# Kernel optimization log

Measured on AMD Instinct MI355X. Metric: run time of the kernel, lower is better.

The kernel has to match this reference:

```python
import jax, jax.numpy as jnp
import numpy as np

N_HEADS = 8


def setup_inputs() -> dict:
    key = jax.random.key(0)
    qkv = jax.random.normal(key, (4, 1536, 2048), dtype=jnp.float32)
    return {"qkv": qkv}


def reference(qkv):
    bs, width, length = qkv.shape
    assert width % (3 * N_HEADS) == 0
    ch = width // (3 * N_HEADS)
    q, k, v = jnp.split(qkv, 3, axis=1)            # each [bs, H*C, T]
    scale = 1.0 / (ch ** 0.25)                      # 1/sqrt(sqrt(ch)) applied to both q and k
    q = (q * scale).reshape(bs * N_HEADS, ch, length)
    k = (k * scale).reshape(bs * N_HEADS, ch, length)
    v = v.reshape(bs * N_HEADS, ch, length)
    weight = jnp.einsum('bct,bcs->bts', q, k)       # [bs*H, T, T]
    weight = jax.nn.softmax(weight.astype(jnp.float32), axis=-1).astype(weight.dtype)
    a = jnp.einsum('bts,bcs->bct', weight, v)       # [bs*H, C, T]
    return a.reshape(bs, -1, length)
```

## Files before the change

### kernel.cpp

```cpp
#include <hip/hip_runtime.h>


typedef _Float16 half8  __attribute__((ext_vector_type(8)));
typedef _Float16 half4  __attribute__((ext_vector_type(4)));
typedef float    floatx4 __attribute__((ext_vector_type(4)));

constexpr int T   = 2048;
constexpr int TQ  = 128;
constexpr int TS  = 64;
constexpr int LDK = 72;
constexpr int LDV = 72;
constexpr int NIT = T / TS;
constexpr float QSCALE = 0.125f * 1.44269504088896340736f;

__device__ __forceinline__ half4 pack4(float a, float b, float c, float d) {
    half4 r;
    r[0] = (_Float16)a; r[1] = (_Float16)b;
    r[2] = (_Float16)c; r[3] = (_Float16)d;
    return r;
}

__global__ __launch_bounds__(512, 4)
void qkv_attn_kernel(const float* __restrict__ qkv, float* __restrict__ out) {
    __shared__ __align__(16) _Float16 sK[2][TS * LDK];
    __shared__ __align__(16) _Float16 sV[2][64 * LDV];

    const int tid  = threadIdx.x;
    const int wave = tid >> 6;
    const int lane = tid & 63;
    const int n16  = lane & 15;
    const int g    = lane >> 4;

    const int bx = blockIdx.x;
    const int h  = bx & 31;
    const int qt = bx >> 5;
    const int b  = h >> 3;
    const int hh = h & 7;
    const int q0 = qt * TQ;

    const float* __restrict__ qbase = qkv + (size_t)(b * 1536 + hh * 64) * T;
    const float* __restrict__ kbase = qkv + (size_t)(b * 1536 + 512 + hh * 64) * T;
    const float* __restrict__ vbase = qkv + (size_t)(b * 1536 + 1024 + hh * 64) * T;
    float* __restrict__ obase = out + (size_t)(b * 512 + hh * 64) * T;

    const bool producer = wave >= 4;

    const int ptid = tid & 255;
    const int ks   = ((ptid >> 6) << 4) | (ptid & 15);
    const int kc4  = ((ptid >> 4) & 3) << 2;
    const int vc   = ptid >> 4;
    const int vs4  = (ptid & 15) << 2;

    auto stage = [&](int buf, int s0) {
        _Float16* kd = &sK[buf][ks * LDK];
        const float* kg = kbase + s0 + ks;
#pragma unroll
        for (int i = 0; i < 4; ++i) {
            const int c = i * 16 + kc4;
            const float f0 = kg[(c + 0) * T];
            const float f1 = kg[(c + 1) * T];
            const float f2 = kg[(c + 2) * T];
            const float f3 = kg[(c + 3) * T];
            *(half4*)&kd[c] = pack4(f0, f1, f2, f3);
        }
        const float* vg = vbase + vc * T + s0 + vs4;
        _Float16* vd = &sV[buf][vc * LDV + vs4];
#pragma unroll
        for (int i = 0; i < 4; ++i) {
            const floatx4 vv = *(const floatx4*)&vg[i * 16 * T];
            *(half4*)&vd[i * 16 * LDV] = pack4(vv.x, vv.y, vv.z, vv.w);
        }
    };

    half8 bq[2][2];
    floatx4 oacc[4][2];
    float lsum[2];

    if (!producer) {
#pragma unroll
        for (int qt2 = 0; qt2 < 2; ++qt2) {
            const int q = q0 + wave * 32 + qt2 * 16 + n16;
#pragma unroll
            for (int kcA = 0; kcA < 2; ++kcA)
#pragma unroll
                for (int j = 0; j < 8; ++j) {
                    const int c = kcA * 32 + g * 8 + j;
                    bq[qt2][kcA][j] = (_Float16)(qbase[c * T + q] * QSCALE);
                }
        }
#pragma unroll
        for (int mt = 0; mt < 4; ++mt)
#pragma unroll
            for (int qt2 = 0; qt2 < 2; ++qt2) oacc[mt][qt2] = (floatx4)(0.f);
        lsum[0] = 0.f; lsum[1] = 0.f;
    }

    if (producer) stage(0, 0);
    __syncthreads();

    for (int it = 0; it < NIT; ++it) {
        const int buf = it & 1;
        if (producer) {
            if (it + 1 < NIT) stage(buf ^ 1, (it + 1) * TS);
        } else {
            const _Float16* kb = &sK[buf][0];
            const _Float16* vb = &sV[buf][0];
#pragma unroll
            for (int kc2 = 0; kc2 < 2; ++kc2) {
                floatx4 sacc[2][2];
#pragma unroll
                for (int sub = 0; sub < 2; ++sub) {
                    const int stile = kc2 * 2 + sub;
                    const half8 ak0 = *(const half8*)&kb[(stile * 16 + n16) * LDK + g * 8];
                    const half8 ak1 = *(const half8*)&kb[(stile * 16 + n16) * LDK + 32 + g * 8];
#pragma unroll
                    for (int qt2 = 0; qt2 < 2; ++qt2) {
                        floatx4 acc = (floatx4)(0.f);
                        acc = __builtin_amdgcn_mfma_f32_16x16x32_f16(ak0, bq[qt2][0], acc, 0, 0, 0);
                        acc = __builtin_amdgcn_mfma_f32_16x16x32_f16(ak1, bq[qt2][1], acc, 0, 0, 0);
                        sacc[qt2][sub] = acc;
                    }
                }
                half8 av[4];
#pragma unroll
                for (int mt = 0; mt < 4; ++mt) {
                    const _Float16* vr = &vb[(mt * 16 + n16) * LDV + kc2 * 32];
                    const half4 lo = *(const half4*)&vr[g * 4];
                    const half4 hi = *(const half4*)&vr[16 + g * 4];
                    av[mt][0] = lo[0]; av[mt][1] = lo[1]; av[mt][2] = lo[2]; av[mt][3] = lo[3];
                    av[mt][4] = hi[0]; av[mt][5] = hi[1]; av[mt][6] = hi[2]; av[mt][7] = hi[3];
                }
#pragma unroll
                for (int qt2 = 0; qt2 < 2; ++qt2) {
                    float pv[8];
#pragma unroll
                    for (int sub = 0; sub < 2; ++sub)
#pragma unroll
                        for (int r = 0; r < 4; ++r)
                            pv[sub * 4 + r] = __builtin_amdgcn_exp2f(sacc[qt2][sub][r]);
                    lsum[qt2] += ((pv[0] + pv[1]) + (pv[2] + pv[3]))
                               + ((pv[4] + pv[5]) + (pv[6] + pv[7]));
                    half8 bp;
#pragma unroll
                    for (int i = 0; i < 8; ++i) bp[i] = (_Float16)pv[i];
#pragma unroll
                    for (int mt = 0; mt < 4; ++mt)
                        oacc[mt][qt2] = __builtin_amdgcn_mfma_f32_16x16x32_f16(
                            av[mt], bp, oacc[mt][qt2], 0, 0, 0);
                }
            }
        }
        __syncthreads();
    }

    if (!producer) {
#pragma unroll
        for (int qt2 = 0; qt2 < 2; ++qt2) {
            float l = lsum[qt2];
            l += __shfl_xor(l, 16);
            l += __shfl_xor(l, 32);
            const float linv = 1.0f / l;
            const int tcol = q0 + wave * 32 + qt2 * 16 + n16;
#pragma unroll
            for (int mt = 0; mt < 4; ++mt)
#pragma unroll
                for (int r = 0; r < 4; ++r)
                    obase[(mt * 16 + g * 4 + r) * T + tcol] = oacc[mt][qt2][r] * linv;
        }
    }
}

extern "C" void kernel_launch(void* const* d_in, const int* in_sizes, int n_in,
                              void* d_out, int out_size, void* d_ws, size_t ws_size,
                              hipStream_t stream) {
    const float* qkv = (const float*)d_in[0];
    float* out = (float*)d_out;
    qkv_attn_kernel<<<dim3(512), dim3(512), 0, stream>>>(qkv, out);
}
```

Measured before the change: 124.7 us.

## Split key tile across all waves and merge partial outputs via shared memory

Replaces the producer/consumer wave split with a scheme where all 8 waves both stage K/V and compute. Each pair of waves shares a query group and takes half of each 64-key tile; the halves are combined through shared memory at the end. Global loads for the next tile are prefetched into registers before compute and written to LDS after it, and the V layout is permuted so each lane reads one contiguous half8. This puts the idle consumer-side waves to work on MFMA, at the cost of more registers per wave and a final LDS reduction.

```diff
diff --git a/kernel.cpp b/kernel.cpp
--- a/kernel.cpp
+++ b/kernel.cpp
@@ -5,12 +5,14 @@
 typedef _Float16 half4  __attribute__((ext_vector_type(4)));
 typedef float    floatx4 __attribute__((ext_vector_type(4)));
 
-constexpr int T   = 2048;
-constexpr int TQ  = 128;
-constexpr int TS  = 64;
-constexpr int LDK = 72;
-constexpr int LDV = 72;
-constexpr int NIT = T / TS;
+constexpr int T    = 2048;
+constexpr int TQ   = 128;
+constexpr int TS   = 64;
+constexpr int LDK  = 72;
+constexpr int LDV  = 72;
+constexpr int KHALF  = TS * LDK;
+constexpr int SMEM_H = KHALF + 64 * LDV;
+constexpr int NIT  = T / TS;
 constexpr float QSCALE = 0.125f * 1.44269504088896340736f;
 
 __device__ __forceinline__ half4 pack4(float a, float b, float c, float d) {
@@ -22,20 +24,21 @@
 
 __global__ __launch_bounds__(512, 4)
 void qkv_attn_kernel(const float* __restrict__ qkv, float* __restrict__ out) {
-    __shared__ __align__(16) _Float16 sK[2][TS * LDK];
-    __shared__ __align__(16) _Float16 sV[2][64 * LDV];
+    __shared__ __align__(16) _Float16 smem[2][SMEM_H];
 
     const int tid  = threadIdx.x;
     const int wave = tid >> 6;
     const int lane = tid & 63;
     const int n16  = lane & 15;
     const int g    = lane >> 4;
+    const int h    = wave >> 2;
+    const int qg   = wave & 3;
 
     const int bx = blockIdx.x;
-    const int h  = bx & 31;
+    const int hd = bx & 31;
     const int qt = bx >> 5;
-    const int b  = h >> 3;
-    const int hh = h & 7;
+    const int b  = hd >> 3;
+    const int hh = hd & 7;
     const int q0 = qt * TQ;
 
     const float* __restrict__ qbase = qkv + (size_t)(b * 1536 + hh * 64) * T;
@@ -43,32 +46,47 @@
     const float* __restrict__ vbase = qkv + (size_t)(b * 1536 + 1024 + hh * 64) * T;
     float* __restrict__ obase = out + (size_t)(b * 512 + hh * 64) * T;
 
-    const bool producer = wave >= 4;
-
+    const bool kstage = (wave < 4);
     const int ptid = tid & 255;
     const int ks   = ((ptid >> 6) << 4) | (ptid & 15);
     const int kc4  = ((ptid >> 4) & 3) << 2;
     const int vc   = ptid >> 4;
-    const int vs4  = (ptid & 15) << 2;
-
-    auto stage = [&](int buf, int s0) {
-        _Float16* kd = &sK[buf][ks * LDK];
-        const float* kg = kbase + s0 + ks;
-#pragma unroll
-        for (int i = 0; i < 4; ++i) {
-            const int c = i * 16 + kc4;
-            const float f0 = kg[(c + 0) * T];
-            const float f1 = kg[(c + 1) * T];
-            const float f2 = kg[(c + 2) * T];
-            const float f3 = kg[(c + 3) * T];
-            *(half4*)&kd[c] = pack4(f0, f1, f2, f3);
-        }
-        const float* vg = vbase + vc * T + s0 + vs4;
-        _Float16* vd = &sV[buf][vc * LDV + vs4];
-#pragma unroll
-        for (int i = 0; i < 4; ++i) {
-            const floatx4 vv = *(const floatx4*)&vg[i * 16 * T];
-            *(half4*)&vd[i * 16 * LDV] = pack4(vv.x, vv.y, vv.z, vv.w);
+    const int vt   = ptid & 15;
+    const int vcol = 32 * (vt >> 3) + 8 * (vt & 3) + 4 * ((vt >> 2) & 1);
+
+    float pre[16];
+    auto prefetch = [&](int s0) {
+        if (kstage) {
+            const float* kg = kbase + s0 + ks;
+#pragma unroll
+            for (int i = 0; i < 4; ++i) {
+                const int c = i * 16 + kc4;
+#pragma unroll
+                for (int j = 0; j < 4; ++j) pre[i * 4 + j] = kg[(c + j) * T];
+            }
+        } else {
+            const float* vg = vbase + vc * T + s0 + vt * 4;
+#pragma unroll
+            for (int i = 0; i < 4; ++i) {
+                const floatx4 vv = *(const floatx4*)&vg[i * 16 * T];
+                pre[i * 4 + 0] = vv.x; pre[i * 4 + 1] = vv.y;
+                pre[i * 4 + 2] = vv.z; pre[i * 4 + 3] = vv.w;
+            }
+        }
+    };
+    auto flush = [&](int buf) {
+        if (kstage) {
+            _Float16* kd = &smem[buf][ks * LDK];
+#pragma unroll
+            for (int i = 0; i < 4; ++i)
+                *(half4*)&kd[i * 16 + kc4] =
+                    pack4(pre[i * 4], pre[i * 4 + 1], pre[i * 4 + 2], pre[i * 4 + 3]);
+        } else {
+            _Float16* vd = &smem[buf][KHALF + vc * LDV + vcol];
+#pragma unroll
+            for (int i = 0; i < 4; ++i)
+                *(half4*)&vd[i * 16 * LDV] =
+                    pack4(pre[i * 4], pre[i * 4 + 1], pre[i * 4 + 2], pre[i * 4 + 3]);
         }
     };
 
@@ -76,91 +94,101 @@
     floatx4 oacc[4][2];
     float lsum[2];
 
-    if (!producer) {
-#pragma unroll
-        for (int qt2 = 0; qt2 < 2; ++qt2) {
-            const int q = q0 + wave * 32 + qt2 * 16 + n16;
-#pragma unroll
-            for (int kcA = 0; kcA < 2; ++kcA)
-#pragma unroll
-                for (int j = 0; j < 8; ++j) {
-                    const int c = kcA * 32 + g * 8 + j;
-                    bq[qt2][kcA][j] = (_Float16)(qbase[c * T + q] * QSCALE);
-                }
-        }
-#pragma unroll
-        for (int mt = 0; mt < 4; ++mt)
-#pragma unroll
-            for (int qt2 = 0; qt2 < 2; ++qt2) oacc[mt][qt2] = (floatx4)(0.f);
-        lsum[0] = 0.f; lsum[1] = 0.f;
-    }
-
-    if (producer) stage(0, 0);
+#pragma unroll
+    for (int qt2 = 0; qt2 < 2; ++qt2) {
+        const int q = q0 + qg * 32 + qt2 * 16 + n16;
+#pragma unroll
+        for (int kcA = 0; kcA < 2; ++kcA)
+#pragma unroll
+            for (int j = 0; j < 8; ++j) {
+                const int c = kcA * 32 + g * 8 + j;
+                bq[qt2][kcA][j] = (_Float16)(qbase[c * T + q] * QSCALE);
+            }
+    }
+#pragma unroll
+    for (int mt = 0; mt < 4; ++mt)
+#pragma unroll
+        for (int qt2 = 0; qt2 < 2; ++qt2) oacc[mt][qt2] = (floatx4)(0.f);
+    lsum[0] = 0.f; lsum[1] = 0.f;
+
+    prefetch(0);
+    flush(0);
     __syncthreads();
 
     for (int it = 0; it < NIT; ++it) {
         const int buf = it & 1;
-        if (producer) {
-            if (it + 1 < NIT) stage(buf ^ 1, (it + 1) * TS);
-        } else {
-            const _Float16* kb = &sK[buf][0];
-            const _Float16* vb = &sV[buf][0];
-#pragma unroll
-            for (int kc2 = 0; kc2 < 2; ++kc2) {
-                floatx4 sacc[2][2];
-#pragma unroll
-                for (int sub = 0; sub < 2; ++sub) {
-                    const int stile = kc2 * 2 + sub;
-                    const half8 ak0 = *(const half8*)&kb[(stile * 16 + n16) * LDK + g * 8];
-                    const half8 ak1 = *(const half8*)&kb[(stile * 16 + n16) * LDK + 32 + g * 8];
-#pragma unroll
-                    for (int qt2 = 0; qt2 < 2; ++qt2) {
-                        floatx4 acc = (floatx4)(0.f);
-                        acc = __builtin_amdgcn_mfma_f32_16x16x32_f16(ak0, bq[qt2][0], acc, 0, 0, 0);
-                        acc = __builtin_amdgcn_mfma_f32_16x16x32_f16(ak1, bq[qt2][1], acc, 0, 0, 0);
-                        sacc[qt2][sub] = acc;
-                    }
-                }
-                half8 av[4];
-#pragma unroll
-                for (int mt = 0; mt < 4; ++mt) {
-                    const _Float16* vr = &vb[(mt * 16 + n16) * LDV + kc2 * 32];
-                    const half4 lo = *(const half4*)&vr[g * 4];
-                    const half4 hi = *(const half4*)&vr[16 + g * 4];
-                    av[mt][0] = lo[0]; av[mt][1] = lo[1]; av[mt][2] = lo[2]; av[mt][3] = lo[3];
-                    av[mt][4] = hi[0]; av[mt][5] = hi[1]; av[mt][6] = hi[2]; av[mt][7] = hi[3];
-                }
-#pragma unroll
-                for (int qt2 = 0; qt2 < 2; ++qt2) {
-                    float pv[8];
-#pragma unroll
-                    for (int sub = 0; sub < 2; ++sub)
-#pragma unroll
-                        for (int r = 0; r < 4; ++r)
-                            pv[sub * 4 + r] = __builtin_amdgcn_exp2f(sacc[qt2][sub][r]);
-                    lsum[qt2] += ((pv[0] + pv[1]) + (pv[2] + pv[3]))
-                               + ((pv[4] + pv[5]) + (pv[6] + pv[7]));
-                    half8 bp;
-#pragma unroll
-                    for (int i = 0; i < 8; ++i) bp[i] = (_Float16)pv[i];
-#pragma unroll
-                    for (int mt = 0; mt < 4; ++mt)
-                        oacc[mt][qt2] = __builtin_amdgcn_mfma_f32_16x16x32_f16(
-                            av[mt], bp, oacc[mt][qt2], 0, 0, 0);
-                }
-            }
-        }
+        if (it + 1 < NIT) prefetch((it + 1) * TS);
+
+        const _Float16* kb = &smem[buf][0];
+        const _Float16* vb = &smem[buf][KHALF];
+
+        floatx4 sacc[2][2];
+#pragma unroll
+        for (int sub = 0; sub < 2; ++sub) {
+            const half8 ak0 = *(const half8*)&kb[((h * 2 + sub) * 16 + n16) * LDK + g * 8];
+            const half8 ak1 = *(const half8*)&kb[((h * 2 + sub) * 16 + n16) * LDK + 32 + g * 8];
+#pragma unroll
+            for (int qt2 = 0; qt2 < 2; ++qt2) {
+                floatx4 acc = (floatx4)(0.f);
+                acc = __builtin_amdgcn_mfma_f32_16x16x32_f16(ak0, bq[qt2][0], acc, 0, 0, 0);
+                acc = __builtin_amdgcn_mfma_f32_16x16x32_f16(ak1, bq[qt2][1], acc, 0, 0, 0);
+                sacc[qt2][sub] = acc;
+            }
+        }
+        half8 av[4];
+#pragma unroll
+        for (int mt = 0; mt < 4; ++mt)
+            av[mt] = *(const half8*)&vb[(mt * 16 + n16) * LDV + h * 32 + g * 8];
+#pragma unroll
+        for (int qt2 = 0; qt2 < 2; ++qt2) {
+            float pv[8];
+#pragma unroll
+            for (int sub = 0; sub < 2; ++sub)
+#pragma unroll
+                for (int r = 0; r < 4; ++r)
+                    pv[sub * 4 + r] = __builtin_amdgcn_exp2f(sacc[qt2][sub][r]);
+            lsum[qt2] += ((pv[0] + pv[1]) + (pv[2] + pv[3]))
+                       + ((pv[4] + pv[5]) + (pv[6] + pv[7]));
+            half8 bp;
+#pragma unroll
+            for (int i = 0; i < 8; ++i) bp[i] = (_Float16)pv[i];
+#pragma unroll
+            for (int mt = 0; mt < 4; ++mt)
+                oacc[mt][qt2] = __builtin_amdgcn_mfma_f32_16x16x32_f16(
+                    av[mt], bp, oacc[mt][qt2], 0, 0, 0);
+        }
+
+        if (it + 1 < NIT) flush(buf ^ 1);
         __syncthreads();
     }
 
-    if (!producer) {
+    float* red = (float*)&smem[0][0];
+    const int rbase = (qg * 64 + lane) * 36;
+    if (h == 1) {
+#pragma unroll
+        for (int qt2 = 0; qt2 < 2; ++qt2)
+#pragma unroll
+            for (int mt = 0; mt < 4; ++mt)
+                *(floatx4*)&red[rbase + (qt2 * 4 + mt) * 4] = oacc[mt][qt2];
+        red[rbase + 32] = lsum[0];
+        red[rbase + 33] = lsum[1];
+    }
+    __syncthreads();
+    if (h == 0) {
+#pragma unroll
+        for (int qt2 = 0; qt2 < 2; ++qt2)
+#pragma unroll
+            for (int mt = 0; mt < 4; ++mt)
+                oacc[mt][qt2] += *(const floatx4*)&red[rbase + (qt2 * 4 + mt) * 4];
+        lsum[0] += red[rbase + 32];
+        lsum[1] += red[rbase + 33];
 #pragma unroll
         for (int qt2 = 0; qt2 < 2; ++qt2) {
             float l = lsum[qt2];
             l += __shfl_xor(l, 16);
             l += __shfl_xor(l, 32);
             const float linv = 1.0f / l;
-            const int tcol = q0 + wave * 32 + qt2 * 16 + n16;
+            const int tcol = q0 + qg * 32 + qt2 * 16 + n16;
 #pragma unroll
             for (int mt = 0; mt < 4; ++mt)
 #pragma unroll
```

New measurement: 124.3 us. Within noise of the previous version (-0.3%).
